# Kernel tuning notes

Hardware: AMD Instinct MI355X
Metric: run time of the kernel (lower is better)

## Reference

```python
import jax, jax.numpy as jnp
import numpy as np

NUM_ITERATIONS = 3


def squash(s, axis=-1):
    # s * sqrt(||s||^2) / (1 + ||s||^2), matching the torch source exactly
    sq = jnp.sum(s * s, axis=axis, keepdims=True)
    return s * jnp.sqrt(sq) / (1.0 + sq)


def setup_inputs() -> dict:
    key = jax.random.key(0)
    k_u, k_w = jax.random.split(key)
    B, J, R, O, I = 128, 166, 864, 8, 4
    u = jax.random.normal(k_u, (B, R, I), dtype=jnp.float32)
    W = jax.random.normal(k_w, (1, J, R, O, I), dtype=jnp.float32)
    return {"u": u, "W": W}


def reference(u, W):
    # u: [B, R, I]; W: [1, J, R, O, I]
    Wq = W[0]  # [J, R, O, I]
    # u_hat[b,j,r,o] = sum_i W[j,r,o,i] * u[b,r,i]
    u_hat = jnp.einsum('jroi,bri->bjro', Wq, u)  # [B, J, R, O]
    # routing logits start shared across batch (torch init: [1,J,R,1,1])
    b_ij = jnp.zeros((1, Wq.shape[0], Wq.shape[1]), dtype=u_hat.dtype)  # [1, J, R]
    v_j = None
    for it in range(NUM_ITERATIONS):
        c_ij = jax.nn.softmax(b_ij, axis=2)           # softmax over routes R
        s_j = jnp.einsum('bjr,bjro->bjo', jnp.broadcast_to(c_ij, u_hat.shape[:3]), u_hat)  # [B, J, O]
        v_j = squash(s_j, axis=-1)                    # [B, J, O]
        if it < NUM_ITERATIONS - 1:
            # agreement a[b,j,r] = <u_hat[b,j,r,:], v[b,j,:]>
            a_ij = jnp.einsum('bjro,bjo->bjr', u_hat, v_j)
            b_ij = b_ij + a_ij                        # broadcasts to [B, J, R]
    return v_j  # equivalent to torch v_j.squeeze() for B > 1
```

## Files before the change

kernel.cpp:

```cpp
#include <hip/hip_runtime.h>
#include <math.h>


#define BB 128
#define JJ 166
#define RR 864
#define OO 8
#define KMAX 14
#define RPAD2 257

typedef __fp16 h2v __attribute__((ext_vector_type(2)));

__device__ __forceinline__ uint32_t pack2(float a, float b) {
    return __builtin_bit_cast(uint32_t, __builtin_amdgcn_cvt_pkrtz(a, b));
}
__device__ __forceinline__ h2v bc_h2(uint32_t u) {
    return __builtin_bit_cast(h2v, u);
}
__device__ __forceinline__ float lo_f(uint32_t u) {
    return (float)__builtin_bit_cast(h2v, u).x;
}
__device__ __forceinline__ float hi_f(uint32_t u) {
    return (float)__builtin_bit_cast(h2v, u).y;
}

__device__ __forceinline__ float wave_sum(float v) {
#pragma unroll
    for (int m = 32; m >= 1; m >>= 1) v += __shfl_xor(v, m, 64);
    return v;
}

__global__ __launch_bounds__(256) void digitcaps_kernel(
    const float* __restrict__ u, const float* __restrict__ W,
    float* __restrict__ out) {
    const int tid = threadIdx.x;
    const int lane = tid & 63;
    const int wave = tid >> 6;

    const int j = blockIdx.x >> 5;
    const int b = ((blockIdx.x & 31) << 2) + wave;

    const float4* __restrict__ u4 = (const float4*)u;
    const float4* __restrict__ W4 = (const float4*)W;

    __shared__ uint2 wlds[2][OO * RPAD2];

    uint32_t uh[KMAX][4];

#define STAGE(CC, BUF, ITERS)                                                  \
    {                                                                          \
        const int gbase = j * (RR * OO) + (CC * 256) * OO;                     \
        _Pragma("unroll")                                                      \
        for (int i = 0; i < (ITERS); ++i) {                                    \
            const int e = tid + (i << 8);                                      \
            const float4 w = W4[gbase + e];                                    \
            wlds[BUF][(e & 7) * RPAD2 + (e >> 3)] =                            \
                make_uint2(pack2(w.x, w.y), pack2(w.z, w.w));                  \
        }                                                                      \
    }

#define COMPUTE(CC, BUF, KK)                                                   \
    {                                                                          \
        _Pragma("unroll")                                                      \
        for (int kl = 0; kl < (KK); ++kl) {                                    \
            const int rl = (kl << 6) + lane;                                   \
            const int r = (CC * 256) + rl;                                     \
            if (r < RR) {                      \
                const float4 uu = u4[b * RR + r];                              \
                const uint32_t up0 = pack2(uu.x, uu.y);                        \
                const uint32_t up1 = pack2(uu.z, uu.w);                        \
                float d[OO];                                                   \
                _Pragma("unroll")                                              \
                for (int o = 0; o < OO; ++o) {                                 \
                    const uint2 ww = wlds[BUF][o * RPAD2 + rl];                \
                    float t = __builtin_amdgcn_fdot2(bc_h2(ww.x), bc_h2(up0),  \
                                                     0.0f, false);             \
                    d[o] = __builtin_amdgcn_fdot2(bc_h2(ww.y), bc_h2(up1), t,  \
                                                  false);                      \
                }                                                              \
                _Pragma("unroll")                                              \
                for (int o2 = 0; o2 < 4; ++o2)                                 \
                    uh[(CC) * 4 + kl][o2] = pack2(d[2 * o2], d[2 * o2 + 1]);   \
            } else {                                                           \
                _Pragma("unroll")                                              \
                for (int o2 = 0; o2 < 4; ++o2) uh[(CC) * 4 + kl][o2] = 0u;     \
            }                                                                  \
        }                                                                      \
    }

    STAGE(0, 0, 8)
    __syncthreads();
    STAGE(1, 1, 8)
    COMPUTE(0, 0, 4)
    __syncthreads();
    STAGE(2, 0, 8)
    COMPUTE(1, 1, 4)
    __syncthreads();
    STAGE(3, 1, 3)
    COMPUTE(2, 0, 4)
    __syncthreads();
    COMPUTE(3, 1, 2)
#undef STAGE
#undef COMPUTE

    float V[OO];
    float v[OO];

    {
        h2v accp[4];
#pragma unroll
        for (int o2 = 0; o2 < 4; ++o2) accp[o2] = bc_h2(uh[0][o2]);
#pragma unroll
        for (int k = 1; k < KMAX; ++k)
#pragma unroll
            for (int o2 = 0; o2 < 4; ++o2) accp[o2] += bc_h2(uh[k][o2]);

        float s[OO];
#pragma unroll
        for (int o2 = 0; o2 < 4; ++o2) {
            s[2 * o2]     = wave_sum((float)accp[o2].x) * (1.0f / (float)RR);
            s[2 * o2 + 1] = wave_sum((float)accp[o2].y) * (1.0f / (float)RR);
        }
        float n2 = 0.0f;
#pragma unroll
        for (int o = 0; o < OO; ++o) n2 += s[o] * s[o];
        const float scale = sqrtf(n2) / (1.0f + n2);
#pragma unroll
        for (int o = 0; o < OO; ++o) { v[o] = s[o] * scale; V[o] = v[o]; }
    }

#pragma unroll
    for (int it = 1; it < 3; ++it) {
        uint32_t Vp[4];
#pragma unroll
        for (int o2 = 0; o2 < 4; ++o2)
            Vp[o2] = pack2(V[2 * o2], V[2 * o2 + 1]);

        float zp = 0.0f;
        float sp[OO];
#pragma unroll
        for (int o = 0; o < OO; ++o) sp[o] = 0.0f;

#pragma unroll
        for (int k = 0; k < KMAX; ++k) {
            float br = 0.0f;
#pragma unroll
            for (int o2 = 0; o2 < 4; ++o2)
                br = __builtin_amdgcn_fdot2(bc_h2(uh[k][o2]), bc_h2(Vp[o2]),
                                            br, false);
            const float e = (k < KMAX - 1 || lane < 32) ? __expf(br) : 0.0f;
            zp += e;
#pragma unroll
            for (int o2 = 0; o2 < 4; ++o2) {
                sp[2 * o2]     = fmaf(e, lo_f(uh[k][o2]), sp[2 * o2]);
                sp[2 * o2 + 1] = fmaf(e, hi_f(uh[k][o2]), sp[2 * o2 + 1]);
            }
        }
        const float invZ = 1.0f / wave_sum(zp);

        float s[OO];
#pragma unroll
        for (int o = 0; o < OO; ++o) s[o] = wave_sum(sp[o]) * invZ;

        float n2 = 0.0f;
#pragma unroll
        for (int o = 0; o < OO; ++o) n2 += s[o] * s[o];
        const float scale = sqrtf(n2) / (1.0f + n2);
#pragma unroll
        for (int o = 0; o < OO; ++o) v[o] = s[o] * scale;

        if (it < 2) {
#pragma unroll
            for (int o = 0; o < OO; ++o) V[o] += v[o];
        }
    }

    float outv = 0.0f;
#pragma unroll
    for (int o = 0; o < OO; ++o)
        if (lane == o) outv = v[o];
    if (lane < OO) out[(b * JJ + j) * OO + lane] = outv;
}

extern "C" void kernel_launch(void* const* d_in, const int* in_sizes, int n_in,
                              void* d_out, int out_size, void* d_ws, size_t ws_size,
                              hipStream_t stream) {
    const float* u = (const float*)d_in[0];
    const float* W = (const float*)d_in[1];
    float* out = (float*)d_out;

    const int grid = JJ * (BB / 4);
    digitcaps_kernel<<<grid, 256, 0, stream>>>(u, W, out);
}
```

Baseline: 144.0 us.

## Prepack W/u to fp16 and recompute u_hat per iteration with lanes over batch

Adds a prepack kernel that converts W and a transposed u to packed fp16 in the workspace. The main kernel now maps 64 batch elements to lanes and splits R across 8 waves. It recomputes u_hat in every routing iteration instead of holding it in registers, and reduces across waves through LDS. Block IDs are remapped for XCD locality and the grid shrinks to 332 blocks of 512 threads. This trades extra arithmetic and a second launch for fewer W loads and smaller register use, at the risk of lower occupancy from the small grid.

```diff
diff --git a/kernel.cpp b/kernel.cpp
--- a/kernel.cpp
+++ b/kernel.cpp
@@ -6,180 +6,194 @@
 #define JJ 166
 #define RR 864
 #define OO 8
-#define KMAX 14
-#define RPAD2 257
+#define W_U2 (JJ * RR * 8)
 
 typedef __fp16 h2v __attribute__((ext_vector_type(2)));
-
-__device__ __forceinline__ uint32_t pack2(float a, float b) {
+typedef float f32x2 __attribute__((ext_vector_type(2)));
+
+static __device__ __forceinline__ uint32_t pack2(float a, float b) {
     return __builtin_bit_cast(uint32_t, __builtin_amdgcn_cvt_pkrtz(a, b));
 }
-__device__ __forceinline__ h2v bc_h2(uint32_t u) {
+static __device__ __forceinline__ h2v bc_h2(uint32_t u) {
     return __builtin_bit_cast(h2v, u);
 }
-__device__ __forceinline__ float lo_f(uint32_t u) {
-    return (float)__builtin_bit_cast(h2v, u).x;
-}
-__device__ __forceinline__ float hi_f(uint32_t u) {
-    return (float)__builtin_bit_cast(h2v, u).y;
-}
-
-__device__ __forceinline__ float wave_sum(float v) {
-#pragma unroll
-    for (int m = 32; m >= 1; m >>= 1) v += __shfl_xor(v, m, 64);
-    return v;
-}
-
-__global__ __launch_bounds__(256) void digitcaps_kernel(
+
+__global__ __launch_bounds__(256) void prepack_kernel(
     const float* __restrict__ u, const float* __restrict__ W,
+    uint2* __restrict__ ws) {
+    const int t = blockIdx.x * 256 + threadIdx.x;
+    if (t < JJ * RR) {
+        const float4* __restrict__ W4 = (const float4*)W + (size_t)t * 8;
+        uint2* __restrict__ dst = ws + (size_t)t * 8;
+#pragma unroll
+        for (int o = 0; o < 8; ++o) {
+            const float4 wv = W4[o];
+            dst[o] = make_uint2(pack2(wv.x, wv.y), pack2(wv.z, wv.w));
+        }
+    } else {
+        const int e = t - JJ * RR;
+        if (e < RR * BB) {
+            const int r = e >> 7;
+            const int b = e & 127;
+            const float4 uu = ((const float4*)u)[(size_t)b * RR + r];
+            ws[W_U2 + e] = make_uint2(pack2(uu.x, uu.y), pack2(uu.z, uu.w));
+        }
+    }
+}
+
+#define UHAT(D)                                                                \
+    {                                                                          \
+        float p;                                                               \
+        p = __builtin_amdgcn_fdot2(bc_h2(w0.x), bc_h2(up.x), 0.0f, false);     \
+        D[0].x = __builtin_amdgcn_fdot2(bc_h2(w0.y), bc_h2(up.y), p, false);   \
+        p = __builtin_amdgcn_fdot2(bc_h2(w0.z), bc_h2(up.x), 0.0f, false);     \
+        D[0].y = __builtin_amdgcn_fdot2(bc_h2(w0.w), bc_h2(up.y), p, false);   \
+        p = __builtin_amdgcn_fdot2(bc_h2(w1.x), bc_h2(up.x), 0.0f, false);     \
+        D[1].x = __builtin_amdgcn_fdot2(bc_h2(w1.y), bc_h2(up.y), p, false);   \
+        p = __builtin_amdgcn_fdot2(bc_h2(w1.z), bc_h2(up.x), 0.0f, false);     \
+        D[1].y = __builtin_amdgcn_fdot2(bc_h2(w1.w), bc_h2(up.y), p, false);   \
+        p = __builtin_amdgcn_fdot2(bc_h2(w2.x), bc_h2(up.x), 0.0f, false);     \
+        D[2].x = __builtin_amdgcn_fdot2(bc_h2(w2.y), bc_h2(up.y), p, false);   \
+        p = __builtin_amdgcn_fdot2(bc_h2(w2.z), bc_h2(up.x), 0.0f, false);     \
+        D[2].y = __builtin_amdgcn_fdot2(bc_h2(w2.w), bc_h2(up.y), p, false);   \
+        p = __builtin_amdgcn_fdot2(bc_h2(w3.x), bc_h2(up.x), 0.0f, false);     \
+        D[3].x = __builtin_amdgcn_fdot2(bc_h2(w3.y), bc_h2(up.y), p, false);   \
+        p = __builtin_amdgcn_fdot2(bc_h2(w3.z), bc_h2(up.x), 0.0f, false);     \
+        D[3].y = __builtin_amdgcn_fdot2(bc_h2(w3.w), bc_h2(up.y), p, false);   \
+    }
+
+#define LOAD_W(T)                                                              \
+    const uint4 w0 = *(const uint4*)(Wr + (T) * 16);                           \
+    const uint4 w1 = *(const uint4*)(Wr + (T) * 16 + 4);                       \
+    const uint4 w2 = *(const uint4*)(Wr + (T) * 16 + 8);                       \
+    const uint4 w3 = *(const uint4*)(Wr + (T) * 16 + 12);
+
+__global__ __launch_bounds__(512) void digitcaps_kernel(
+    const uint32_t* __restrict__ Wp,
+    const uint2* __restrict__ uT,
     float* __restrict__ out) {
     const int tid = threadIdx.x;
-    const int lane = tid & 63;
-    const int wave = tid >> 6;
-
-    const int j = blockIdx.x >> 5;
-    const int b = ((blockIdx.x & 31) << 2) + wave;
-
-    const float4* __restrict__ u4 = (const float4*)u;
-    const float4* __restrict__ W4 = (const float4*)W;
-
-    __shared__ uint2 wlds[2][OO * RPAD2];
-
-    uint32_t uh[KMAX][4];
-
-#define STAGE(CC, BUF, ITERS)                                                  \
-    {                                                                          \
-        const int gbase = j * (RR * OO) + (CC * 256) * OO;                     \
-        _Pragma("unroll")                                                      \
-        for (int i = 0; i < (ITERS); ++i) {                                    \
-            const int e = tid + (i << 8);                                      \
-            const float4 w = W4[gbase + e];                                    \
-            wlds[BUF][(e & 7) * RPAD2 + (e >> 3)] =                            \
-                make_uint2(pack2(w.x, w.y), pack2(w.z, w.w));                  \
-        }                                                                      \
-    }
-
-#define COMPUTE(CC, BUF, KK)                                                   \
-    {                                                                          \
-        _Pragma("unroll")                                                      \
-        for (int kl = 0; kl < (KK); ++kl) {                                    \
-            const int rl = (kl << 6) + lane;                                   \
-            const int r = (CC * 256) + rl;                                     \
-            if (r < RR) {                      \
-                const float4 uu = u4[b * RR + r];                              \
-                const uint32_t up0 = pack2(uu.x, uu.y);                        \
-                const uint32_t up1 = pack2(uu.z, uu.w);                        \
-                float d[OO];                                                   \
-                _Pragma("unroll")                                              \
-                for (int o = 0; o < OO; ++o) {                                 \
-                    const uint2 ww = wlds[BUF][o * RPAD2 + rl];                \
-                    float t = __builtin_amdgcn_fdot2(bc_h2(ww.x), bc_h2(up0),  \
-                                                     0.0f, false);             \
-                    d[o] = __builtin_amdgcn_fdot2(bc_h2(ww.y), bc_h2(up1), t,  \
-                                                  false);                      \
-                }                                                              \
-                _Pragma("unroll")                                              \
-                for (int o2 = 0; o2 < 4; ++o2)                                 \
-                    uh[(CC) * 4 + kl][o2] = pack2(d[2 * o2], d[2 * o2 + 1]);   \
-            } else {                                                           \
-                _Pragma("unroll")                                              \
-                for (int o2 = 0; o2 < 4; ++o2) uh[(CC) * 4 + kl][o2] = 0u;     \
-            }                                                                  \
-        }                                                                      \
-    }
-
-    STAGE(0, 0, 8)
-    __syncthreads();
-    STAGE(1, 1, 8)
-    COMPUTE(0, 0, 4)
-    __syncthreads();
-    STAGE(2, 0, 8)
-    COMPUTE(1, 1, 4)
-    __syncthreads();
-    STAGE(3, 1, 3)
-    COMPUTE(2, 0, 4)
-    __syncthreads();
-    COMPUTE(3, 1, 2)
-#undef STAGE
-#undef COMPUTE
-
-    float V[OO];
-    float v[OO];
+    const int l = tid & 63;
+    const int w = __builtin_amdgcn_readfirstlane(tid >> 6);
+
+    const int orig = blockIdx.x;
+    const int xcd = orig & 7;
+    const int q = 332 / 8, rm = 332 % 8;
+    const int base =
+        (xcd < rm) ? xcd * (q + 1) : rm * (q + 1) + (xcd - rm) * q;
+    const int bid = base + (orig >> 3);
+
+    const int j = bid >> 1;
+    const int b = ((bid & 1) << 6) + l;
+
+    const int r0 = w * 108;
+    const uint32_t* __restrict__ Wr = Wp + ((size_t)j * RR + r0) * 16;
+    const uint2* __restrict__ ur = uT + (size_t)r0 * BB + b;
+
+    __shared__ float4 xA[8 * 64];
+    __shared__ float4 xB[8 * 64];
+    __shared__ float xZ[8 * 64];
+
+    f32x2 V2[4], v2[4];
 
     {
-        h2v accp[4];
-#pragma unroll
-        for (int o2 = 0; o2 < 4; ++o2) accp[o2] = bc_h2(uh[0][o2]);
-#pragma unroll
-        for (int k = 1; k < KMAX; ++k)
-#pragma unroll
-            for (int o2 = 0; o2 < 4; ++o2) accp[o2] += bc_h2(uh[k][o2]);
-
-        float s[OO];
-#pragma unroll
-        for (int o2 = 0; o2 < 4; ++o2) {
-            s[2 * o2]     = wave_sum((float)accp[o2].x) * (1.0f / (float)RR);
-            s[2 * o2 + 1] = wave_sum((float)accp[o2].y) * (1.0f / (float)RR);
-        }
-        float n2 = 0.0f;
-#pragma unroll
-        for (int o = 0; o < OO; ++o) n2 += s[o] * s[o];
+        f32x2 s2[4];
+#pragma unroll
+        for (int k = 0; k < 4; ++k) { s2[k].x = 0.f; s2[k].y = 0.f; }
+#pragma unroll 2
+        for (int t = 0; t < 108; ++t) {
+            const uint2 up = ur[t * BB];
+            LOAD_W(t)
+            f32x2 d2[4];
+            UHAT(d2)
+#pragma unroll
+            for (int k = 0; k < 4; ++k) s2[k] += d2[k];
+        }
+        xA[w * 64 + l] = make_float4(s2[0].x, s2[0].y, s2[1].x, s2[1].y);
+        xB[w * 64 + l] = make_float4(s2[2].x, s2[2].y, s2[3].x, s2[3].y);
+        __syncthreads();
+        float4 A = xA[l], B = xB[l];
+#pragma unroll
+        for (int w2i = 1; w2i < 8; ++w2i) {
+            const float4 a2 = xA[w2i * 64 + l], b2 = xB[w2i * 64 + l];
+            A.x += a2.x; A.y += a2.y; A.z += a2.z; A.w += a2.w;
+            B.x += b2.x; B.y += b2.y; B.z += b2.z; B.w += b2.w;
+        }
+        __syncthreads();
+        const float inv = 1.0f / (float)RR;
+        f32x2 sc[4];
+        sc[0].x = A.x * inv; sc[0].y = A.y * inv;
+        sc[1].x = A.z * inv; sc[1].y = A.w * inv;
+        sc[2].x = B.x * inv; sc[2].y = B.y * inv;
+        sc[3].x = B.z * inv; sc[3].y = B.w * inv;
+        float n2 = 0.f;
+#pragma unroll
+        for (int k = 0; k < 4; ++k) n2 += sc[k].x * sc[k].x + sc[k].y * sc[k].y;
         const float scale = sqrtf(n2) / (1.0f + n2);
 #pragma unroll
-        for (int o = 0; o < OO; ++o) { v[o] = s[o] * scale; V[o] = v[o]; }
+        for (int k = 0; k < 4; ++k) { v2[k] = sc[k] * scale; V2[k] = v2[k]; }
     }
 
 #pragma unroll
     for (int it = 1; it < 3; ++it) {
-        uint32_t Vp[4];
-#pragma unroll
-        for (int o2 = 0; o2 < 4; ++o2)
-            Vp[o2] = pack2(V[2 * o2], V[2 * o2 + 1]);
-
-        float zp = 0.0f;
-        float sp[OO];
-#pragma unroll
-        for (int o = 0; o < OO; ++o) sp[o] = 0.0f;
-
-#pragma unroll
-        for (int k = 0; k < KMAX; ++k) {
-            float br = 0.0f;
-#pragma unroll
-            for (int o2 = 0; o2 < 4; ++o2)
-                br = __builtin_amdgcn_fdot2(bc_h2(uh[k][o2]), bc_h2(Vp[o2]),
-                                            br, false);
-            const float e = (k < KMAX - 1 || lane < 32) ? __expf(br) : 0.0f;
-            zp += e;
-#pragma unroll
-            for (int o2 = 0; o2 < 4; ++o2) {
-                sp[2 * o2]     = fmaf(e, lo_f(uh[k][o2]), sp[2 * o2]);
-                sp[2 * o2 + 1] = fmaf(e, hi_f(uh[k][o2]), sp[2 * o2 + 1]);
-            }
-        }
-        const float invZ = 1.0f / wave_sum(zp);
-
-        float s[OO];
-#pragma unroll
-        for (int o = 0; o < OO; ++o) s[o] = wave_sum(sp[o]) * invZ;
-
-        float n2 = 0.0f;
-#pragma unroll
-        for (int o = 0; o < OO; ++o) n2 += s[o] * s[o];
+        f32x2 sz2[4];
+        float z = 0.f;
+#pragma unroll
+        for (int k = 0; k < 4; ++k) { sz2[k].x = 0.f; sz2[k].y = 0.f; }
+#pragma unroll 2
+        for (int t = 0; t < 108; ++t) {
+            const uint2 up = ur[t * BB];
+            LOAD_W(t)
+            f32x2 d2[4];
+            UHAT(d2)
+            f32x2 lac = d2[0] * V2[0];
+            lac += d2[1] * V2[1];
+            lac += d2[2] * V2[2];
+            lac += d2[3] * V2[3];
+            const float br = lac.x + lac.y;
+            const float e = __expf(br);
+            z += e;
+            f32x2 e2; e2.x = e; e2.y = e;
+#pragma unroll
+            for (int k = 0; k < 4; ++k) sz2[k] += e2 * d2[k];
+        }
+        xA[w * 64 + l] = make_float4(sz2[0].x, sz2[0].y, sz2[1].x, sz2[1].y);
+        xB[w * 64 + l] = make_float4(sz2[2].x, sz2[2].y, sz2[3].x, sz2[3].y);
+        xZ[w * 64 + l] = z;
+        __syncthreads();
+        float4 A = xA[l], B = xB[l];
+        float Z = xZ[l];
+#pragma unroll
+        for (int w2i = 1; w2i < 8; ++w2i) {
+            const float4 a2 = xA[w2i * 64 + l], b2 = xB[w2i * 64 + l];
+            A.x += a2.x; A.y += a2.y; A.z += a2.z; A.w += a2.w;
+            B.x += b2.x; B.y += b2.y; B.z += b2.z; B.w += b2.w;
+            Z += xZ[w2i * 64 + l];
+        }
+        __syncthreads();
+        const float invZ = 1.0f / Z;
+        f32x2 sc[4];
+        sc[0].x = A.x * invZ; sc[0].y = A.y * invZ;
+        sc[1].x = A.z * invZ; sc[1].y = A.w * invZ;
+        sc[2].x = B.x * invZ; sc[2].y = B.y * invZ;
+        sc[3].x = B.z * invZ; sc[3].y = B.w * invZ;
+        float n2 = 0.f;
+#pragma unroll
+        for (int k = 0; k < 4; ++k) n2 += sc[k].x * sc[k].x + sc[k].y * sc[k].y;
         const float scale = sqrtf(n2) / (1.0f + n2);
 #pragma unroll
-        for (int o = 0; o < OO; ++o) v[o] = s[o] * scale;
-
-        if (it < 2) {
-#pragma unroll
-            for (int o = 0; o < OO; ++o) V[o] += v[o];
-        }
-    }
-
-    float outv = 0.0f;
-#pragma unroll
-    for (int o = 0; o < OO; ++o)
-        if (lane == o) outv = v[o];
-    if (lane < OO) out[(b * JJ + j) * OO + lane] = outv;
+        for (int k = 0; k < 4; ++k) v2[k] = sc[k] * scale;
+        if (it == 1) {
+#pragma unroll
+            for (int k = 0; k < 4; ++k) V2[k] += v2[k];
+        }
+    }
+
+    if (w == 0) {
+        float4* dst = (float4*)(out + ((size_t)b * JJ + j) * OO);
+        dst[0] = make_float4(v2[0].x, v2[0].y, v2[1].x, v2[1].y);
+        dst[1] = make_float4(v2[2].x, v2[2].y, v2[3].x, v2[3].y);
+    }
 }
 
 extern "C" void kernel_launch(void* const* d_in, const int* in_sizes, int n_in,
@@ -188,7 +202,11 @@
     const float* u = (const float*)d_in[0];
     const float* W = (const float*)d_in[1];
     float* out = (float*)d_out;
-
-    const int grid = JJ * (BB / 4);
-    digitcaps_kernel<<<grid, 256, 0, stream>>>(u, W, out);
-}
+    uint2* ws = (uint2*)d_ws;
+
+    const int total = JJ * RR + RR * BB;
+    prepack_kernel<<<(total + 255) / 256, 256, 0, stream>>>(u, W, ws);
+
+    digitcaps_kernel<<<JJ * 2, 512, 0, stream>>>(
+        (const uint32_t*)ws, ((const uint2*)ws) + W_U2, out);
+}
```

Measured after the change: 162.7 us. 1.13x slower.
